# Kernel optimization log

Hardware: AMD Instinct MI355X
Metric: run time of the kernel (lower is better)

## Reference

```python
import jax, jax.numpy as jnp
import numpy as np

B, T, HID = 1, 8192, 2048
NH, NKV, D = 32, 8, 64
BLK, LOCAL, GLOB = 64, 8, 1
THETA = 10000.0
SCALE = 1.0 / float(np.sqrt(D))
NEG = -1e9


def _sparse_tables(nb):
    """Replicates HumanVAttention._get_sparse_tables: per query block i select
    global blocks [0, GLOB) then local blocks [i-LOCAL+1, i], dedup keeping order."""
    max_sel = LOCAL + GLOB
    idx = np.zeros((nb, max_sel), np.int32)
    valid = np.zeros((nb, max_sel), bool)
    for i in range(nb):
        sel = [g for g in range(GLOB) if g < nb]
        sel += list(range(max(0, i - (LOCAL - 1)), i + 1))
        li, seen = [], set()
        for x in sel:
            if x not in seen:
                li.append(x); seen.add(x)
        idx[i, :len(li)] = li
        valid[i, :len(li)] = True
    return idx, valid


def _rotate_half(x):
    x1, x2 = x[..., : x.shape[-1] // 2], x[..., x.shape[-1] // 2:]
    return jnp.concatenate((-x2, x1), axis=-1)


def setup_inputs() -> dict:
    key = jax.random.key(0)
    ks = jax.random.split(key, 5)
    s = 0.02
    return {
        "hidden_states": jax.random.normal(ks[0], (B, T, HID), jnp.float32),
        "Wq": jax.random.normal(ks[1], (NH * D, HID), jnp.float32) * s,
        "Wk": jax.random.normal(ks[2], (NKV * D, HID), jnp.float32) * s,
        "Wv": jax.random.normal(ks[3], (NKV * D, HID), jnp.float32) * s,
        "Wo": jax.random.normal(ks[4], (NH * D, NH * D), jnp.float32) * s,
    }


def reference(hidden_states, Wq, Wk, Wv, Wo):
    hs = hidden_states
    # projections (nn.Linear: y = x @ W.T)
    q = (hs @ Wq.T).reshape(B, T, NH, D).transpose(0, 2, 1, 3)     # [B,NH,T,D]
    k = (hs @ Wk.T).reshape(B, T, NKV, D).transpose(0, 2, 1, 3)    # [B,NKV,T,D]
    v = (hs @ Wv.T).reshape(B, T, NKV, D).transpose(0, 2, 1, 3)

    # RoPE (full rotary factor)
    inv = 1.0 / (THETA ** (jnp.arange(0, D, 2, dtype=jnp.float32) / D))
    fr = jnp.arange(T, dtype=jnp.float32)[:, None] * inv[None, :]  # [T,D/2]
    emb = jnp.concatenate([fr, fr], axis=-1)                       # [T,D]
    cos = jnp.cos(emb)[None, None]                                 # [1,1,T,D]
    sin = jnp.sin(emb)[None, None]
    q = q * cos + _rotate_half(q) * sin
    k = k * cos + _rotate_half(k) * sin

    nb = T // BLK
    G = NH // NKV
    idx_np, valid_np = _sparse_tables(nb)
    max_sel = idx_np.shape[1]

    # gather selected K/V blocks per query block
    kb = k.reshape(B, NKV, nb, BLK, D)
    vb = v.reshape(B, NKV, nb, BLK, D)
    idx = jnp.asarray(idx_np)
    k_sel = kb[:, :, idx].reshape(B, NKV, nb, max_sel * BLK, D)    # [B,NKV,nb,M,D]
    v_sel = vb[:, :, idx].reshape(B, NKV, nb, max_sel * BLK, D)

    qg = q.reshape(B, NKV, G, nb, BLK, D)                          # grouped queries
    scores = jnp.einsum('bkgnqd,bknmd->bkgnqm',
                        qg.astype(jnp.float32), k_sel.astype(jnp.float32)) * SCALE

    # causal + validity mask over selected keys (static, built in numpy)
    kpos = (idx_np[:, :, None] * BLK + np.arange(BLK)).reshape(nb, -1)   # [nb,M]
    qpos = np.arange(nb)[:, None] * BLK + np.arange(BLK)                 # [nb,BLK]
    valid_flat = np.repeat(valid_np, BLK, axis=1)                        # [nb,M]
    allowed = valid_flat[:, None, :] & (kpos[:, None, :] <= qpos[:, :, None])
    scores = jnp.where(jnp.asarray(allowed)[None, None, None], scores, NEG)

    probs = jax.nn.softmax(scores, axis=-1)
    out = jnp.einsum('bkgnqm,bknmd->bkgnqd', probs.astype(v.dtype), v_sel)
    out = out.astype(hs.dtype).reshape(B, NH, T, D).transpose(0, 2, 1, 3)
    out = out.reshape(B, T, NH * D)
    return out @ Wo.T
```

## Files before the change

### kernel.cpp

```cpp
#include <hip/hip_runtime.h>
#include <cstdint>
#include <cstddef>

typedef __bf16 bf16;
typedef __attribute__((ext_vector_type(8))) __bf16 bf16x8;
typedef __attribute__((ext_vector_type(4))) __bf16 bf16x4;
typedef __attribute__((ext_vector_type(4))) float f32x4;

#define ATT_SCALE 0.125f
#define NEG_BIG  -1000000000.0f

__device__ __forceinline__ f32x4 mfma16(bf16x8 a, bf16x8 b, f32x4 c) {
  return __builtin_amdgcn_mfma_f32_16x16x32_bf16(a, b, c, 0, 0, 0);
}

__device__ __forceinline__ void gload16(const bf16* g, bf16* l) {
  __builtin_amdgcn_global_load_lds((__attribute__((address_space(1))) void*)g,
                                   (__attribute__((address_space(3))) void*)l,
                                   16, 0, 0);
}

__global__ __launch_bounds__(256) void prep_all(const float* __restrict__ hs,
                                                const float* __restrict__ Wq,
                                                const float* __restrict__ Wk,
                                                const float* __restrict__ Wv,
                                                const float* __restrict__ Wo,
                                                bf16* __restrict__ hs16, bf16* __restrict__ wq16,
                                                bf16* __restrict__ wk16, bf16* __restrict__ wv16,
                                                bf16* __restrict__ wo16,
                                                float* __restrict__ cosT, float* __restrict__ sinT) {
  int b = blockIdx.x, t = threadIdx.x;
  const float* src; bf16* dst; int i;
  if (b < 16384)      { src = hs; dst = hs16; i = b * 256 + t; }
  else if (b < 20480) { src = Wq; dst = wq16; i = (b - 16384) * 256 + t; }
  else if (b < 21504) { src = Wk; dst = wk16; i = (b - 20480) * 256 + t; }
  else if (b < 22528) { src = Wv; dst = wv16; i = (b - 21504) * 256 + t; }
  else if (b < 26624) { src = Wo; dst = wo16; i = (b - 22528) * 256 + t; }
  else {
    int idx = (b - 26624) * 256 + t;
    int tt = idx >> 5, j = idx & 31;
    float inv = exp2f(-(float)j * (13.287712379549449f / 32.0f));
    float fr = (float)tt * inv;
    cosT[idx] = cosf(fr); sinT[idx] = sinf(fr);
    return;
  }
  float4 v = *((const float4*)src + i);
  bf16x4 o;
  o[0] = (bf16)v.x; o[1] = (bf16)v.y; o[2] = (bf16)v.z; o[3] = (bf16)v.w;
  *((bf16x4*)dst + i) = o;
}

template <int BSEL, int OUTF32, int ROPE>
__global__ __launch_bounds__(512, 2) void gemm256(const bf16* __restrict__ A,
                                                  const bf16* __restrict__ B0,
                                                  const bf16* __restrict__ B1,
                                                  const bf16* __restrict__ B2,
                                                  void* __restrict__ Cout,
                                                  const float* __restrict__ cosT,
                                                  const float* __restrict__ sinT,
                                                  int N, int K) {
  __shared__ bf16 Asm[4][8192];
  __shared__ bf16 Bsm[4][8192];
  const int tid = threadIdx.x, lane = tid & 63, wid = tid >> 6;
  const int m0 = blockIdx.x * 256, n0 = blockIdx.y * 256;
  const int wr = wid >> 2, wc = wid & 3;
  const int fr = lane & 15, g4 = lane >> 4;
  const int sw8 = (g4 ^ ((fr >> 1) & 3)) * 8;

  f32x4 acc[8][4] = {};

  auto brow = [&](int n) -> const bf16* {
    if (BSEL) {
      if (n < 2048) return B0 + (size_t)n * K;
      if (n < 2560) return B1 + (size_t)(n - 2048) * K;
      return B2 + (size_t)(n - 2560) * K;
    }
    return B0 + (size_t)n * K;
  };

  const bf16* aS0; const bf16* aS1; const bf16* bS0; const bf16* bS1;
  {
    int c0 = tid, r0 = c0 >> 2, l0 = (c0 & 3) ^ ((r0 >> 1) & 3);
    int c1 = 512 + tid, r1 = c1 >> 2, l1 = (c1 & 3) ^ ((r1 >> 1) & 3);
    aS0 = A + (size_t)(m0 + r0) * K + l0 * 8;
    aS1 = A + (size_t)(m0 + r1) * K + l1 * 8;
    bS0 = brow(n0 + r0) + l0 * 8;
    bS1 = brow(n0 + r1) + l1 * 8;
  }
  const int dst0 = (wid * 64) * 8;
  const int dst1 = (512 + wid * 64) * 8;

#define STAGE_A(kt) { bf16* d = &Asm[(kt) & 3][0]; \
    gload16(aS0 + (kt) * 32, d + dst0); gload16(aS1 + (kt) * 32, d + dst1); }
#define STAGE_B(kt) { bf16* d = &Bsm[(kt) & 3][0]; \
    gload16(bS0 + (kt) * 32, d + dst0); gload16(bS1 + (kt) * 32, d + dst1); }

#define KTILE(kt, VM, STG) { \
    asm volatile("s_waitcnt vmcnt(" VM ")" ::: "memory"); \
    __builtin_amdgcn_s_barrier(); \
    __builtin_amdgcn_sched_barrier(0); \
    const bf16* Ab = &Asm[(kt) & 3][0]; \
    const bf16* Bb = &Bsm[(kt) & 3][0]; \
    bf16x8 bfr[4], af[4]; \
    _Pragma("unroll") for (int nf = 0; nf < 4; ++nf) \
      bfr[nf] = *(const bf16x8*)(Bb + (wc * 64 + nf * 16 + fr) * 32 + sw8); \
    _Pragma("unroll") for (int mf = 0; mf < 4; ++mf) \
      af[mf] = *(const bf16x8*)(Ab + (wr * 128 + mf * 16 + fr) * 32 + sw8); \
    if (STG) STAGE_A((kt) + 3); \
    __builtin_amdgcn_s_setprio(1); \
    _Pragma("unroll") for (int mf = 0; mf < 4; ++mf) \
      _Pragma("unroll") for (int nf = 0; nf < 4; ++nf) \
        acc[mf][nf] = mfma16(af[mf], bfr[nf], acc[mf][nf]); \
    __builtin_amdgcn_s_setprio(0); \
    _Pragma("unroll") for (int mf = 0; mf < 4; ++mf) \
      af[mf] = *(const bf16x8*)(Ab + (wr * 128 + 64 + mf * 16 + fr) * 32 + sw8); \
    if (STG) STAGE_B((kt) + 3); \
    __builtin_amdgcn_s_setprio(1); \
    _Pragma("unroll") for (int mf = 0; mf < 4; ++mf) \
      _Pragma("unroll") for (int nf = 0; nf < 4; ++nf) \
        acc[4 + mf][nf] = mfma16(af[mf], bfr[nf], acc[4 + mf][nf]); \
    __builtin_amdgcn_s_setprio(0); \
  }

  STAGE_A(0); STAGE_B(0);
  STAGE_A(1); STAGE_B(1);
  STAGE_A(2); STAGE_B(2);

  const int NT = K >> 5;
  for (int kt = 0; kt < NT - 3; ++kt) KTILE(kt, "8", 1);
  KTILE(NT - 3, "8", 0);
  KTILE(NT - 2, "4", 0);
  KTILE(NT - 1, "0", 0);
#undef KTILE
#undef STAGE_A
#undef STAGE_B

  const int fc = lane & 15, fr4 = (lane >> 4) * 4;
  if (ROPE && (n0 + wc * 64) < 2560) {
#pragma unroll
    for (int am = 0; am < 8; ++am)
#pragma unroll
      for (int i = 0; i < 4; ++i) {
        size_t row = (size_t)(m0 + wr * 128 + am * 16 + fr4 + i);
        bf16* base = (bf16*)Cout + row * (size_t)N + n0 + wc * 64;
#pragma unroll
        for (int nf = 0; nf < 2; ++nf) {
          int j = nf * 16 + fc;
          float c = cosT[row * 32 + j], sn = sinT[row * 32 + j];
          float x1 = acc[am][nf][i], x2 = acc[am][nf + 2][i];
          base[j]      = (bf16)(x1 * c - x2 * sn);
          base[j + 32] = (bf16)(x2 * c + x1 * sn);
        }
      }
  } else {
#pragma unroll
    for (int am = 0; am < 8; ++am)
#pragma unroll
      for (int i = 0; i < 4; ++i) {
        size_t row = (size_t)(m0 + wr * 128 + am * 16 + fr4 + i);
#pragma unroll
        for (int nf = 0; nf < 4; ++nf) {
          int col = n0 + wc * 64 + nf * 16 + fc;
          if (OUTF32)
            ((float*)Cout)[row * (size_t)N + col] = acc[am][nf][i];
          else
            ((bf16*)Cout)[row * (size_t)N + col] = (bf16)acc[am][nf][i];
        }
      }
  }
}

__global__ __launch_bounds__(1024) void attn_sparse(const bf16* __restrict__ qkv,
                                                    bf16* __restrict__ attn) {
  const int iblk = blockIdx.x;
  const int kv = blockIdx.y;
  const int tid = threadIdx.x, lane = tid & 63, wid = tid >> 6;
  const int hloc = wid >> 2;
  const int h = kv * 4 + hloc;
  const int rg = wid & 3;

  __shared__ bf16 Ks[64 * 64];
  __shared__ bf16 Vt[2][64 * 72];
  __shared__ bf16 Ps[16 * 16 * 68];

  const int qcol = h * 64, kcol = 2048 + kv * 64, vcol = 2560 + kv * 64;
  const size_t trow0 = (size_t)iblk * 64;
  const int fr = lane & 15, g4 = lane >> 4, fk = g4 * 8, fr4 = g4 * 4;

  const bf16* qrow = qkv + (trow0 + rg * 16 + fr) * 3072 + qcol;
  bf16x8 bq0 = *(const bf16x8*)(qrow + fk);
  bf16x8 bq1 = *(const bf16x8*)(qrow + 32 + fk);

  float mrun = -INFINITY, lrun = 0.f;
  f32x4 acc[4] = {};

  const int kr = tid >> 3, ks = tid & 7;
  const int vu = tid & 511, vp = vu & 31, vd0 = (vu >> 5) * 4;
  const bool isK = (tid < 512);

  const int nsel = (iblk < 8) ? (iblk + 1) : 9;
  auto jof = [&](int js) { return (iblk < 8) ? js : ((js == 0) ? 0 : iblk - 8 + js); };

  {
    const size_t krow = (size_t)jof(0) * 64;
    if (isK) {
      const bf16* src = qkv + (krow + kr) * 3072 + kcol + ((ks ^ (kr & 7)) * 8);
      gload16(src, Ks + (tid >> 6) * 512);
    } else {
      const bf16* v0p = qkv + (krow + 2 * vp) * 3072 + vcol + vd0;
      uint64_t a = *(const uint64_t*)v0p;
      uint64_t b = *(const uint64_t*)(v0p + 3072);
#pragma unroll
      for (int e = 0; e < 4; ++e) {
        uint32_t w = (uint32_t)((a >> (16 * e)) & 0xFFFF) |
                     ((uint32_t)((b >> (16 * e)) & 0xFFFF) << 16);
        *(uint32_t*)(&Vt[0][0] + (vd0 + e) * 72 + 2 * vp) = w;
      }
    }
  }
  __syncthreads();

  for (int js = 0; js < nsel; ++js) {
    const int cur = js & 1;
    const int jblk = jof(js);
    const bool pre = (js + 1 < nsel);

    uint64_t va = 0, vb2 = 0;
    if (pre && !isK) {
      const bf16* v0p = qkv + ((size_t)jof(js + 1) * 64 + 2 * vp) * 3072 + vcol + vd0;
      va = *(const uint64_t*)v0p;
      vb2 = *(const uint64_t*)(v0p + 3072);
    }

    f32x4 s[4];
#pragma unroll
    for (int n = 0; n < 4; ++n) {
      const char* krowp = (const char*)Ks + (n * 16 + fr) * 128;
      bf16x8 kb0 = *(const bf16x8*)(krowp + ((g4 ^ (fr & 7)) << 4));
      bf16x8 kb1 = *(const bf16x8*)(krowp + (((4 + g4) ^ (fr & 7)) << 4));
      f32x4 z = {};
      z = mfma16(kb0, bq0, z);
      s[n] = mfma16(kb1, bq1, z);
    }

    __syncthreads();
    if (pre && isK) {
      const bf16* src = qkv + ((size_t)jof(js + 1) * 64 + kr) * 3072 + kcol +
                        ((ks ^ (kr & 7)) * 8);
      gload16(src, Ks + (tid >> 6) * 512);
    }

    const bool diag = (jblk == iblk);
    const int qr = rg * 16 + fr;
#pragma unroll
    for (int n = 0; n < 4; ++n)
#pragma unroll
      for (int i = 0; i < 4; ++i) {
        float sv = s[n][i] * ATT_SCALE;
        if (diag && (n * 16 + fr4 + i) > qr) sv = NEG_BIG;
        s[n][i] = sv;
      }

    float t0 = fmaxf(fmaxf(s[0][0], s[0][1]), fmaxf(s[0][2], s[0][3]));
    float t1 = fmaxf(fmaxf(s[1][0], s[1][1]), fmaxf(s[1][2], s[1][3]));
    float t2 = fmaxf(fmaxf(s[2][0], s[2][1]), fmaxf(s[2][2], s[2][3]));
    float t3 = fmaxf(fmaxf(s[3][0], s[3][1]), fmaxf(s[3][2], s[3][3]));
    float mx = fmaxf(fmaxf(t0, t1), fmaxf(t2, t3));
    mx = fmaxf(mx, __shfl_xor(mx, 16, 64));
    mx = fmaxf(mx, __shfl_xor(mx, 32, 64));
    float mnew = fmaxf(mrun, mx);
    float corr = __expf(mrun - mnew);
    mrun = mnew;
    float ps = 0.f;
#pragma unroll
    for (int n = 0; n < 4; ++n) {
      float p0 = __expf(s[n][0] - mnew), p1 = __expf(s[n][1] - mnew);
      float p2 = __expf(s[n][2] - mnew), p3 = __expf(s[n][3] - mnew);
      s[n][0] = p0; s[n][1] = p1; s[n][2] = p2; s[n][3] = p3;
      ps += (p0 + p1) + (p2 + p3);
    }
    ps += __shfl_xor(ps, 16, 64);
    ps += __shfl_xor(ps, 32, 64);
    lrun = lrun * corr + ps;

    float cq[4];
#pragma unroll
    for (int i = 0; i < 4; ++i) cq[i] = __shfl(corr, fr4 + i, 64);
#pragma unroll
    for (int n = 0; n < 4; ++n)
#pragma unroll
      for (int i = 0; i < 4; ++i) acc[n][i] *= cq[i];

    bf16* pbase = Ps + wid * (16 * 68);
#pragma unroll
    for (int n = 0; n < 4; ++n) {
      bf16x4 pk;
#pragma unroll
      for (int i = 0; i < 4; ++i) pk[i] = (bf16)s[n][i];
      *(bf16x4*)(pbase + fr * 68 + n * 16 + fr4) = pk;
    }
    bf16x8 pa0 = *(const bf16x8*)(pbase + fr * 68 + fk);
    bf16x8 pa1 = *(const bf16x8*)(pbase + fr * 68 + 32 + fk);

    if (pre && !isK) {
#pragma unroll
      for (int e = 0; e < 4; ++e) {
        uint32_t w = (uint32_t)((va >> (16 * e)) & 0xFFFF) |
                     ((uint32_t)((vb2 >> (16 * e)) & 0xFFFF) << 16);
        *(uint32_t*)(&Vt[cur ^ 1][0] + (vd0 + e) * 72 + 2 * vp) = w;
      }
    }

#pragma unroll
    for (int n = 0; n < 4; ++n) {
      bf16x8 vb0 = *(const bf16x8*)(&Vt[cur][0] + (n * 16 + fr) * 72 + fk);
      bf16x8 vb1 = *(const bf16x8*)(&Vt[cur][0] + (n * 16 + fr) * 72 + 32 + fk);
      acc[n] = mfma16(pa0, vb0, acc[n]);
      acc[n] = mfma16(pa1, vb1, acc[n]);
    }
    __syncthreads();
  }

  float lq[4];
#pragma unroll
  for (int i = 0; i < 4; ++i) lq[i] = __shfl(lrun, fr4 + i, 64);
#pragma unroll
  for (int i = 0; i < 4; ++i) {
    float rl = 1.0f / lq[i];
    size_t t = trow0 + rg * 16 + fr4 + i;
#pragma unroll
    for (int n = 0; n < 4; ++n)
      attn[t * 2048 + h * 64 + n * 16 + fr] = (bf16)(acc[n][i] * rl);
  }
}

extern "C" void kernel_launch(void* const* d_in, const int* in_sizes, int n_in,
                              void* d_out, int out_size, void* d_ws, size_t ws_size,
                              hipStream_t stream) {
  (void)in_sizes; (void)n_in; (void)out_size; (void)ws_size;
  const float* hs = (const float*)d_in[0];
  const float* Wq = (const float*)d_in[1];
  const float* Wk = (const float*)d_in[2];
  const float* Wv = (const float*)d_in[3];
  const float* Wo = (const float*)d_in[4];
  float* out = (float*)d_out;

  char* ws = (char*)d_ws;
  bf16* hs16 = (bf16*)(ws + 0);
  bf16* qkv  = (bf16*)(ws + 33554432);
  bf16* attn = (bf16*)(ws + 83886080);
  bf16* wq16 = (bf16*)(ws + 117440512);
  bf16* wk16 = (bf16*)(ws + 125829120);
  bf16* wv16 = (bf16*)(ws + 127926272);
  bf16* wo16 = (bf16*)(ws + 130023424);
  float* cosT = (float*)(ws + 138412032);
  float* sinT = (float*)(ws + 139460608);

  prep_all<<<27648, 256, 0, stream>>>(hs, Wq, Wk, Wv, Wo,
                                      hs16, wq16, wk16, wv16, wo16, cosT, sinT);

  gemm256<1, 0, 1><<<dim3(32, 12), 512, 0, stream>>>(hs16, wq16, wk16, wv16, qkv,
                                                     cosT, sinT, 3072, 2048);
  attn_sparse<<<dim3(128, 8), 1024, 0, stream>>>(qkv, attn);
  gemm256<0, 1, 0><<<dim3(32, 8), 512, 0, stream>>>(attn, wo16, wo16, wo16, out,
                                                    nullptr, nullptr, 2048, 2048);
}
```

Baseline: 319.4 us.

## Restructure GEMM mainloop into ping-pong double-buffered phases with XCD-aware block remap

Changes the 256x256 GEMM main loop from a 4-stage ring of K=32 tiles into two K=64 buffers, each split into two K halves. The work runs as eight phases per 128-wide K step, each with a barrier, a single global-to-LDS stage, and 16 MFMAs, with explicit lgkmcnt/vmcnt waits. It also remaps the linear block id so consecutive tiles are spread across the eight XCDs, which is meant to improve L2 locality. The extra barriers per phase could add sync overhead, and the remap assumes the tile count divides by 8.

```diff
diff --git a/kernel.cpp b/kernel.cpp
--- a/kernel.cpp
+++ b/kernel.cpp
@@ -59,10 +59,16 @@
                                                   const float* __restrict__ cosT,
                                                   const float* __restrict__ sinT,
                                                   int N, int K) {
-  __shared__ bf16 Asm[4][8192];
-  __shared__ bf16 Bsm[4][8192];
+  __shared__ bf16 As[2][2][8192];
+  __shared__ bf16 Bs[2][2][8192];
   const int tid = threadIdx.x, lane = tid & 63, wid = tid >> 6;
-  const int m0 = blockIdx.x * 256, n0 = blockIdx.y * 256;
+
+  const int nx = gridDim.x;
+  int lin = blockIdx.x + nx * blockIdx.y;
+  const int cpx = (nx * gridDim.y) >> 3;
+  lin = (lin & 7) * cpx + (lin >> 3);
+  const int m0 = (lin % nx) * 256, n0 = (lin / nx) * 256;
+
   const int wr = wid >> 2, wc = wid & 3;
   const int fr = lane & 15, g4 = lane >> 4;
   const int sw8 = (g4 ^ ((fr >> 1) & 3)) * 8;
@@ -78,60 +84,79 @@
     return B0 + (size_t)n * K;
   };
 
-  const bf16* aS0; const bf16* aS1; const bf16* bS0; const bf16* bS1;
-  {
-    int c0 = tid, r0 = c0 >> 2, l0 = (c0 & 3) ^ ((r0 >> 1) & 3);
-    int c1 = 512 + tid, r1 = c1 >> 2, l1 = (c1 & 3) ^ ((r1 >> 1) & 3);
-    aS0 = A + (size_t)(m0 + r0) * K + l0 * 8;
-    aS1 = A + (size_t)(m0 + r1) * K + l1 * 8;
-    bS0 = brow(n0 + r0) + l0 * 8;
-    bS1 = brow(n0 + r1) + l1 * 8;
-  }
-  const int dst0 = (wid * 64) * 8;
-  const int dst1 = (512 + wid * 64) * 8;
-
-#define STAGE_A(kt) { bf16* d = &Asm[(kt) & 3][0]; \
-    gload16(aS0 + (kt) * 32, d + dst0); gload16(aS1 + (kt) * 32, d + dst1); }
-#define STAGE_B(kt) { bf16* d = &Bsm[(kt) & 3][0]; \
-    gload16(bS0 + (kt) * 32, d + dst0); gload16(bS1 + (kt) * 32, d + dst1); }
-
-#define KTILE(kt, VM, STG) { \
-    asm volatile("s_waitcnt vmcnt(" VM ")" ::: "memory"); \
+  const int r0 = tid >> 2, r1 = 128 + (tid >> 2);
+  const int l0 = (tid & 3) ^ ((r0 >> 1) & 3);
+  const int l1 = (tid & 3) ^ ((r1 >> 1) & 3);
+  const bf16* aS0 = A + (size_t)(m0 + r0) * K + l0 * 8;
+  const bf16* aS1 = A + (size_t)(m0 + r1) * K + l1 * 8;
+  const bf16* bS0 = brow(n0 + r0) + l0 * 8;
+  const bf16* bS1 = brow(n0 + r1) + l1 * 8;
+  const int st0 = wid * 512;
+  const int st1 = 4096 + wid * 512;
+
+#define STAGE_A(BUF, KH, KT) { \
+    gload16(aS0 + (KT) * 64 + (KH) * 32, &As[BUF][KH][0] + st0); \
+    gload16(aS1 + (KT) * 64 + (KH) * 32, &As[BUF][KH][0] + st1); }
+#define STAGE_B(BUF, KH, KT) { \
+    gload16(bS0 + (KT) * 64 + (KH) * 32, &Bs[BUF][KH][0] + st0); \
+    gload16(bS1 + (KT) * 64 + (KH) * 32, &Bs[BUF][KH][0] + st1); }
+#define VMX {}
+#define VM4 { asm volatile("s_waitcnt vmcnt(4)" ::: "memory"); }
+#define VM0 { asm volatile("s_waitcnt vmcnt(0)" ::: "memory"); }
+
+#define PHASE(BUF, KK, MH, LOADB, STG, VM) { \
+    if (LOADB) { \
+      _Pragma("unroll") for (int nf = 0; nf < 4; ++nf) \
+        bfr[nf] = *(const bf16x8*)(&Bs[BUF][KK][0] + (wc * 64 + nf * 16 + fr) * 32 + sw8); \
+    } \
+    bf16x8 af[4]; \
+    _Pragma("unroll") for (int mf = 0; mf < 4; ++mf) \
+      af[mf] = *(const bf16x8*)(&As[BUF][KK][0] + (wr * 128 + (MH) * 64 + mf * 16 + fr) * 32 + sw8); \
+    STG \
     __builtin_amdgcn_s_barrier(); \
+    asm volatile("s_waitcnt lgkmcnt(0)" ::: "memory"); \
     __builtin_amdgcn_sched_barrier(0); \
-    const bf16* Ab = &Asm[(kt) & 3][0]; \
-    const bf16* Bb = &Bsm[(kt) & 3][0]; \
-    bf16x8 bfr[4], af[4]; \
-    _Pragma("unroll") for (int nf = 0; nf < 4; ++nf) \
-      bfr[nf] = *(const bf16x8*)(Bb + (wc * 64 + nf * 16 + fr) * 32 + sw8); \
-    _Pragma("unroll") for (int mf = 0; mf < 4; ++mf) \
-      af[mf] = *(const bf16x8*)(Ab + (wr * 128 + mf * 16 + fr) * 32 + sw8); \
-    if (STG) STAGE_A((kt) + 3); \
     __builtin_amdgcn_s_setprio(1); \
     _Pragma("unroll") for (int mf = 0; mf < 4; ++mf) \
       _Pragma("unroll") for (int nf = 0; nf < 4; ++nf) \
-        acc[mf][nf] = mfma16(af[mf], bfr[nf], acc[mf][nf]); \
+        acc[(MH) * 4 + mf][nf] = mfma16(af[mf], bfr[nf], acc[(MH) * 4 + mf][nf]); \
     __builtin_amdgcn_s_setprio(0); \
-    _Pragma("unroll") for (int mf = 0; mf < 4; ++mf) \
-      af[mf] = *(const bf16x8*)(Ab + (wr * 128 + 64 + mf * 16 + fr) * 32 + sw8); \
-    if (STG) STAGE_B((kt) + 3); \
-    __builtin_amdgcn_s_setprio(1); \
-    _Pragma("unroll") for (int mf = 0; mf < 4; ++mf) \
-      _Pragma("unroll") for (int nf = 0; nf < 4; ++nf) \
-        acc[4 + mf][nf] = mfma16(af[mf], bfr[nf], acc[4 + mf][nf]); \
-    __builtin_amdgcn_s_setprio(0); \
-  }
-
-  STAGE_A(0); STAGE_B(0);
-  STAGE_A(1); STAGE_B(1);
-  STAGE_A(2); STAGE_B(2);
-
-  const int NT = K >> 5;
-  for (int kt = 0; kt < NT - 3; ++kt) KTILE(kt, "8", 1);
-  KTILE(NT - 3, "8", 0);
-  KTILE(NT - 2, "4", 0);
-  KTILE(NT - 1, "0", 0);
-#undef KTILE
+    VM \
+    __builtin_amdgcn_s_barrier(); \
+    __builtin_amdgcn_sched_barrier(0); }
+
+  STAGE_A(0, 0, 0); STAGE_B(0, 0, 0);
+  STAGE_A(0, 1, 0); STAGE_B(0, 1, 0);
+  STAGE_A(1, 0, 1); STAGE_B(1, 0, 1);
+  asm volatile("s_waitcnt vmcnt(4)" ::: "memory");
+  __builtin_amdgcn_s_barrier();
+
+  const int NI = K >> 7;
+  for (int i = 0; i < NI - 1; ++i) {
+    const int kt = 2 * i;
+    bf16x8 bfr[4];
+    PHASE(0, 0, 0, 1, STAGE_A(1, 1, kt + 1), VMX)
+    PHASE(0, 0, 1, 0, STAGE_B(1, 1, kt + 1), VM4)
+    PHASE(0, 1, 0, 1, STAGE_A(0, 0, kt + 2), VMX)
+    PHASE(0, 1, 1, 0, STAGE_B(0, 0, kt + 2), VM4)
+    PHASE(1, 0, 0, 1, STAGE_A(0, 1, kt + 2), VMX)
+    PHASE(1, 0, 1, 0, STAGE_B(0, 1, kt + 2), VM4)
+    PHASE(1, 1, 0, 1, STAGE_A(1, 0, kt + 3), VMX)
+    PHASE(1, 1, 1, 0, STAGE_B(1, 0, kt + 3), VM4)
+  }
+  {
+    const int kt = 2 * (NI - 1);
+    bf16x8 bfr[4];
+    PHASE(0, 0, 0, 1, STAGE_A(1, 1, kt + 1), VMX)
+    PHASE(0, 0, 1, 0, STAGE_B(1, 1, kt + 1), VM4)
+    PHASE(0, 1, 0, 1, {}, VMX)
+    PHASE(0, 1, 1, 0, {}, VM0)
+    PHASE(1, 0, 0, 1, {}, VMX)
+    PHASE(1, 0, 1, 0, {}, VMX)
+    PHASE(1, 1, 0, 1, {}, VMX)
+    PHASE(1, 1, 1, 0, {}, VMX)
+  }
+#undef PHASE
 #undef STAGE_A
 #undef STAGE_B
 
@@ -141,7 +166,7 @@
     for (int am = 0; am < 8; ++am)
 #pragma unroll
       for (int i = 0; i < 4; ++i) {
-        size_t row = (size_t)(m0 + wr * 128 + am * 16 + fr4 + i);
+        size_t row = (size_t)(m0 + wr * 128 + (am >> 2) * 64 + (am & 3) * 16 + fr4 + i);
         bf16* base = (bf16*)Cout + row * (size_t)N + n0 + wc * 64;
 #pragma unroll
         for (int nf = 0; nf < 2; ++nf) {
@@ -157,7 +182,7 @@
     for (int am = 0; am < 8; ++am)
 #pragma unroll
       for (int i = 0; i < 4; ++i) {
-        size_t row = (size_t)(m0 + wr * 128 + am * 16 + fr4 + i);
+        size_t row = (size_t)(m0 + wr * 128 + (am >> 2) * 64 + (am & 3) * 16 + fr4 + i);
 #pragma unroll
         for (int nf = 0; nf < 4; ++nf) {
           int col = n0 + wc * 64 + nf * 16 + fc;
```

After: 362.2 us. 13.4% more time.

## Load GEMM B operand directly into registers, dropping its LDS staging

Applied to the files above, without the earlier changes.

The B tile is no longer staged through shared memory with async global-to-LDS loads. Each wave now loads its B fragments straight from global memory into double-buffered registers, one k-tile ahead. Only A stays in the 4-stage LDS ring. This halves LDS footprint and LDS traffic, which could allow higher occupancy. The cost is that B reuse across waves is lost: each wave row re-reads the same B columns from global or L2. Prefetching only one tile ahead may also expose load latency, and the vmcnt accounting changes.

```diff
diff --git a/kernel.cpp b/kernel.cpp
--- a/kernel.cpp
+++ b/kernel.cpp
@@ -59,10 +59,10 @@
                                                   const float* __restrict__ cosT,
                                                   const float* __restrict__ sinT,
                                                   int N, int K) {
-  __shared__ bf16 Asm[4][8192];
-  __shared__ bf16 Bsm[4][8192];
+  __shared__ bf16 As[4][8192];
   const int tid = threadIdx.x, lane = tid & 63, wid = tid >> 6;
   const int m0 = blockIdx.x * 256, n0 = blockIdx.y * 256;
+
   const int wr = wid >> 2, wc = wid & 3;
   const int fr = lane & 15, g4 = lane >> 4;
   const int sw8 = (g4 ^ ((fr >> 1) & 3)) * 8;
@@ -78,62 +78,67 @@
     return B0 + (size_t)n * K;
   };
 
-  const bf16* aS0; const bf16* aS1; const bf16* bS0; const bf16* bS1;
-  {
-    int c0 = tid, r0 = c0 >> 2, l0 = (c0 & 3) ^ ((r0 >> 1) & 3);
-    int c1 = 512 + tid, r1 = c1 >> 2, l1 = (c1 & 3) ^ ((r1 >> 1) & 3);
-    aS0 = A + (size_t)(m0 + r0) * K + l0 * 8;
-    aS1 = A + (size_t)(m0 + r1) * K + l1 * 8;
-    bS0 = brow(n0 + r0) + l0 * 8;
-    bS1 = brow(n0 + r1) + l1 * 8;
-  }
-  const int dst0 = (wid * 64) * 8;
-  const int dst1 = (512 + wid * 64) * 8;
-
-#define STAGE_A(kt) { bf16* d = &Asm[(kt) & 3][0]; \
-    gload16(aS0 + (kt) * 32, d + dst0); gload16(aS1 + (kt) * 32, d + dst1); }
-#define STAGE_B(kt) { bf16* d = &Bsm[(kt) & 3][0]; \
-    gload16(bS0 + (kt) * 32, d + dst0); gload16(bS1 + (kt) * 32, d + dst1); }
-
-#define KTILE(kt, VM, STG) { \
+  const int r0 = tid >> 2, r1 = 128 + (tid >> 2);
+  const int l0 = (tid & 3) ^ ((r0 >> 1) & 3);
+  const int l1 = (tid & 3) ^ ((r1 >> 1) & 3);
+  const bf16* aS0 = A + (size_t)(m0 + r0) * K + l0 * 8;
+  const bf16* aS1 = A + (size_t)(m0 + r1) * K + l1 * 8;
+  const int st0 = wid * 512;
+  const int st1 = 4096 + wid * 512;
+
+  const bf16* bp[4];
+#pragma unroll
+  for (int nf = 0; nf < 4; ++nf)
+    bp[nf] = brow(n0 + wc * 64 + nf * 16 + fr) + g4 * 8;
+
+  bf16x8 bA[4], bB[4];
+
+#define STAGE_A(KT) { \
+    gload16(aS0 + (KT) * 32, &As[(KT) & 3][0] + st0); \
+    gload16(aS1 + (KT) * 32, &As[(KT) & 3][0] + st1); }
+
+#define TILE(KT, BCUR, BNXT, VM, STG, PF) { \
     asm volatile("s_waitcnt vmcnt(" VM ")" ::: "memory"); \
     __builtin_amdgcn_s_barrier(); \
     __builtin_amdgcn_sched_barrier(0); \
-    const bf16* Ab = &Asm[(kt) & 3][0]; \
-    const bf16* Bb = &Bsm[(kt) & 3][0]; \
-    bf16x8 bfr[4], af[4]; \
-    _Pragma("unroll") for (int nf = 0; nf < 4; ++nf) \
-      bfr[nf] = *(const bf16x8*)(Bb + (wc * 64 + nf * 16 + fr) * 32 + sw8); \
+    const bf16* Ab = &As[(KT) & 3][0]; \
+    bf16x8 af[4]; \
     _Pragma("unroll") for (int mf = 0; mf < 4; ++mf) \
       af[mf] = *(const bf16x8*)(Ab + (wr * 128 + mf * 16 + fr) * 32 + sw8); \
-    if (STG) STAGE_A((kt) + 3); \
+    if (PF) { _Pragma("unroll") for (int nf = 0; nf < 4; ++nf) \
+      BNXT[nf] = *(const bf16x8*)(bp[nf] + ((KT) + 1) * 32); } \
+    if (STG) STAGE_A((KT) + 3); \
     __builtin_amdgcn_s_setprio(1); \
     _Pragma("unroll") for (int mf = 0; mf < 4; ++mf) \
       _Pragma("unroll") for (int nf = 0; nf < 4; ++nf) \
-        acc[mf][nf] = mfma16(af[mf], bfr[nf], acc[mf][nf]); \
+        acc[mf][nf] = mfma16(af[mf], BCUR[nf], acc[mf][nf]); \
     __builtin_amdgcn_s_setprio(0); \
     _Pragma("unroll") for (int mf = 0; mf < 4; ++mf) \
       af[mf] = *(const bf16x8*)(Ab + (wr * 128 + 64 + mf * 16 + fr) * 32 + sw8); \
-    if (STG) STAGE_B((kt) + 3); \
     __builtin_amdgcn_s_setprio(1); \
     _Pragma("unroll") for (int mf = 0; mf < 4; ++mf) \
       _Pragma("unroll") for (int nf = 0; nf < 4; ++nf) \
-        acc[4 + mf][nf] = mfma16(af[mf], bfr[nf], acc[4 + mf][nf]); \
+        acc[4 + mf][nf] = mfma16(af[mf], BCUR[nf], acc[4 + mf][nf]); \
     __builtin_amdgcn_s_setprio(0); \
   }
 
-  STAGE_A(0); STAGE_B(0);
-  STAGE_A(1); STAGE_B(1);
-  STAGE_A(2); STAGE_B(2);
+  STAGE_A(0);
+#pragma unroll
+  for (int nf = 0; nf < 4; ++nf) bA[nf] = *(const bf16x8*)(bp[nf]);
+  STAGE_A(1);
+  STAGE_A(2);
 
   const int NT = K >> 5;
-  for (int kt = 0; kt < NT - 3; ++kt) KTILE(kt, "8", 1);
-  KTILE(NT - 3, "8", 0);
-  KTILE(NT - 2, "4", 0);
-  KTILE(NT - 1, "0", 0);
-#undef KTILE
+  TILE(0, bA, bB, "4", 1, 1)
+  for (int kt = 1; kt + 2 < NT - 1; kt += 2) {
+    TILE(kt, bB, bA, "2", 1, 1)
+    TILE(kt + 1, bA, bB, "2", 1, 1)
+  }
+  TILE(NT - 3, bB, bA, "2", 0, 1)
+  TILE(NT - 2, bA, bB, "0", 0, 1)
+  TILE(NT - 1, bB, bA, "0", 0, 0)
+#undef TILE
 #undef STAGE_A
-#undef STAGE_B
 
   const int fc = lane & 15, fr4 = (lane >> 4) * 4;
   if (ROPE && (n0 + wc * 64) < 2560) {
```

Result: slower. 425.6 us (+33.2%).

## Use 256x384 tiles with triple buffering for fused QKV GEMM

Applied to the files above, without the earlier changes.

The QKV projection now runs in a dedicated kernel with 256x384 output tiles, so the grid is 32x8 = 256 blocks instead of 384. That matches one wave of blocks on the 256 CUs and removes the partial second wave. Each block uses a 2x4 warp layout with 64x192 per warp and a 3-stage LDS ring buffer instead of 4 stages, with RoPE applied per 64-column group in the epilogue. The output projection becomes a specialised non-template copy of the old GEMM. The cost is more accumulator registers per thread (48 f32x4) and the loss of the two-blocks-per-CU launch bound, which lowers occupancy.

```diff
diff --git a/kernel.cpp b/kernel.cpp
--- a/kernel.cpp
+++ b/kernel.cpp
@@ -50,33 +50,137 @@
   *((bf16x4*)dst + i) = o;
 }
 
-template <int BSEL, int OUTF32, int ROPE>
-__global__ __launch_bounds__(512, 2) void gemm256(const bf16* __restrict__ A,
-                                                  const bf16* __restrict__ B0,
-                                                  const bf16* __restrict__ B1,
-                                                  const bf16* __restrict__ B2,
-                                                  void* __restrict__ Cout,
-                                                  const float* __restrict__ cosT,
-                                                  const float* __restrict__ sinT,
-                                                  int N, int K) {
-  __shared__ bf16 Asm[4][8192];
-  __shared__ bf16 Bsm[4][8192];
+__global__ __launch_bounds__(512) void gemm_qkv(const bf16* __restrict__ A,
+                                                const bf16* __restrict__ B0,
+                                                const bf16* __restrict__ B1,
+                                                const bf16* __restrict__ B2,
+                                                bf16* __restrict__ C,
+                                                const float* __restrict__ cosT,
+                                                const float* __restrict__ sinT) {
+  __shared__ bf16 As[3][8192];
+  __shared__ bf16 Bs[3][12288];
+  const int tid = threadIdx.x, lane = tid & 63, wid = tid >> 6;
+  const int m0 = blockIdx.x * 256, n0 = blockIdx.y * 384;
+  const int wr = wid >> 1, wc = wid & 1;
+  const int fr = lane & 15, g4 = lane >> 4;
+  const int sw8 = (g4 ^ ((fr >> 1) & 3)) * 8;
+
+  f32x4 acc[4][12] = {};
+
+  auto brow = [&](int n) -> const bf16* {
+    if (n < 2048) return B0 + (size_t)n * 2048;
+    if (n < 2560) return B1 + (size_t)(n - 2048) * 2048;
+    return B2 + (size_t)(n - 2560) * 2048;
+  };
+
+  const int ra0 = tid >> 2, ra1 = 128 + (tid >> 2), rb2r = 256 + (tid >> 2);
+  const bf16* aS0 = A + (size_t)(m0 + ra0) * 2048 + ((tid & 3) ^ ((ra0 >> 1) & 3)) * 8;
+  const bf16* aS1 = A + (size_t)(m0 + ra1) * 2048 + ((tid & 3) ^ ((ra1 >> 1) & 3)) * 8;
+  const bf16* bS0 = brow(n0 + ra0) + ((tid & 3) ^ ((ra0 >> 1) & 3)) * 8;
+  const bf16* bS1 = brow(n0 + ra1) + ((tid & 3) ^ ((ra1 >> 1) & 3)) * 8;
+  const bf16* bS2 = brow(n0 + rb2r) + ((tid & 3) ^ ((rb2r >> 1) & 3)) * 8;
+  const int d0 = wid * 512, d1 = 4096 + wid * 512, d2 = 8192 + wid * 512;
+
+#define STQA(BS, KT)  { bf16* d = &As[BS][0]; \
+    gload16(aS0 + (KT) * 32, d + d0); gload16(aS1 + (KT) * 32, d + d1); }
+#define STQB0(BS, KT) { bf16* d = &Bs[BS][0]; \
+    gload16(bS0 + (KT) * 32, d + d0); gload16(bS1 + (KT) * 32, d + d1); }
+#define STQB1(BS, KT) { gload16(bS2 + (KT) * 32, &Bs[BS][0] + d2); }
+
+#define QTILE(KT, BI, BS, VM, STG) { \
+    asm volatile("s_waitcnt vmcnt(" VM ")" ::: "memory"); \
+    __builtin_amdgcn_s_barrier(); \
+    __builtin_amdgcn_sched_barrier(0); \
+    const bf16* Ab = &As[BI][0]; \
+    const bf16* Bb = &Bs[BI][0]; \
+    bf16x8 af[4], bfr[4]; \
+    _Pragma("unroll") for (int mf = 0; mf < 4; ++mf) \
+      af[mf] = *(const bf16x8*)(Ab + (wr * 64 + mf * 16 + fr) * 32 + sw8); \
+    _Pragma("unroll") for (int q = 0; q < 4; ++q) \
+      bfr[q] = *(const bf16x8*)(Bb + (wc * 192 + q * 16 + fr) * 32 + sw8); \
+    if (STG) STQA(BS, (KT) + 2); \
+    __builtin_amdgcn_s_setprio(1); \
+    _Pragma("unroll") for (int mf = 0; mf < 4; ++mf) \
+      _Pragma("unroll") for (int q = 0; q < 4; ++q) \
+        acc[mf][q] = mfma16(af[mf], bfr[q], acc[mf][q]); \
+    __builtin_amdgcn_s_setprio(0); \
+    _Pragma("unroll") for (int q = 0; q < 4; ++q) \
+      bfr[q] = *(const bf16x8*)(Bb + (wc * 192 + 64 + q * 16 + fr) * 32 + sw8); \
+    if (STG) STQB0(BS, (KT) + 2); \
+    __builtin_amdgcn_s_setprio(1); \
+    _Pragma("unroll") for (int mf = 0; mf < 4; ++mf) \
+      _Pragma("unroll") for (int q = 0; q < 4; ++q) \
+        acc[mf][4 + q] = mfma16(af[mf], bfr[q], acc[mf][4 + q]); \
+    __builtin_amdgcn_s_setprio(0); \
+    _Pragma("unroll") for (int q = 0; q < 4; ++q) \
+      bfr[q] = *(const bf16x8*)(Bb + (wc * 192 + 128 + q * 16 + fr) * 32 + sw8); \
+    if (STG) STQB1(BS, (KT) + 2); \
+    __builtin_amdgcn_s_setprio(1); \
+    _Pragma("unroll") for (int mf = 0; mf < 4; ++mf) \
+      _Pragma("unroll") for (int q = 0; q < 4; ++q) \
+        acc[mf][8 + q] = mfma16(af[mf], bfr[q], acc[mf][8 + q]); \
+    __builtin_amdgcn_s_setprio(0); \
+  }
+
+  STQA(0, 0); STQB0(0, 0); STQB1(0, 0);
+  STQA(1, 1); STQB0(1, 1); STQB1(1, 1);
+
+  int bi = 0, bs = 2;
+  for (int kt = 0; kt < 62; ++kt) {
+    QTILE(kt, bi, bs, "5", 1)
+    bi = (bi == 2) ? 0 : bi + 1;
+    bs = (bs == 2) ? 0 : bs + 1;
+  }
+  QTILE(62, bi, bs, "5", 0)
+  bi = (bi == 2) ? 0 : bi + 1;
+  QTILE(63, bi, bi, "0", 0)
+#undef QTILE
+#undef STQA
+#undef STQB0
+#undef STQB1
+
+  const int fc = lane & 15, fr4 = (lane >> 4) * 4;
+#pragma unroll
+  for (int mf = 0; mf < 4; ++mf)
+#pragma unroll
+    for (int i = 0; i < 4; ++i) {
+      size_t row = (size_t)(m0 + wr * 64 + mf * 16 + fr4 + i);
+      bf16* base = C + row * 3072 + n0 + wc * 192;
+      const float* cr = cosT + row * 32;
+      const float* sr = sinT + row * 32;
+#pragma unroll
+      for (int g = 0; g < 3; ++g) {
+        if (n0 + wc * 192 + g * 64 < 2560) {
+#pragma unroll
+          for (int q = 0; q < 2; ++q) {
+            int j = q * 16 + fc;
+            float c = cr[j], sn = sr[j];
+            float x1 = acc[mf][g * 4 + q][i], x2 = acc[mf][g * 4 + q + 2][i];
+            base[g * 64 + j]      = (bf16)(x1 * c - x2 * sn);
+            base[g * 64 + j + 32] = (bf16)(x2 * c + x1 * sn);
+          }
+        } else {
+#pragma unroll
+          for (int q = 0; q < 4; ++q)
+            base[g * 64 + q * 16 + fc] = (bf16)acc[mf][g * 4 + q][i];
+        }
+      }
+    }
+}
+
+__global__ __launch_bounds__(512, 2) void gemm_out(const bf16* __restrict__ A,
+                                                   const bf16* __restrict__ B0,
+                                                   float* __restrict__ Cout) {
+  __shared__ bf16 As[4][8192];
+  __shared__ bf16 Bs[4][8192];
   const int tid = threadIdx.x, lane = tid & 63, wid = tid >> 6;
   const int m0 = blockIdx.x * 256, n0 = blockIdx.y * 256;
   const int wr = wid >> 2, wc = wid & 3;
   const int fr = lane & 15, g4 = lane >> 4;
   const int sw8 = (g4 ^ ((fr >> 1) & 3)) * 8;
+  const int K = 2048, N = 2048;
 
   f32x4 acc[8][4] = {};
-
-  auto brow = [&](int n) -> const bf16* {
-    if (BSEL) {
-      if (n < 2048) return B0 + (size_t)n * K;
-      if (n < 2560) return B1 + (size_t)(n - 2048) * K;
-      return B2 + (size_t)(n - 2560) * K;
-    }
-    return B0 + (size_t)n * K;
-  };
 
   const bf16* aS0; const bf16* aS1; const bf16* bS0; const bf16* bS1;
   {
@@ -84,29 +188,29 @@
     int c1 = 512 + tid, r1 = c1 >> 2, l1 = (c1 & 3) ^ ((r1 >> 1) & 3);
     aS0 = A + (size_t)(m0 + r0) * K + l0 * 8;
     aS1 = A + (size_t)(m0 + r1) * K + l1 * 8;
-    bS0 = brow(n0 + r0) + l0 * 8;
-    bS1 = brow(n0 + r1) + l1 * 8;
-  }
-  const int dst0 = (wid * 64) * 8;
-  const int dst1 = (512 + wid * 64) * 8;
-
-#define STAGE_A(kt) { bf16* d = &Asm[(kt) & 3][0]; \
-    gload16(aS0 + (kt) * 32, d + dst0); gload16(aS1 + (kt) * 32, d + dst1); }
-#define STAGE_B(kt) { bf16* d = &Bsm[(kt) & 3][0]; \
-    gload16(bS0 + (kt) * 32, d + dst0); gload16(bS1 + (kt) * 32, d + dst1); }
-
-#define KTILE(kt, VM, STG) { \
+    bS0 = B0 + (size_t)(n0 + r0) * K + l0 * 8;
+    bS1 = B0 + (size_t)(n0 + r1) * K + l1 * 8;
+  }
+  const int dst0 = wid * 512;
+  const int dst1 = 4096 + wid * 512;
+
+#define STAGE_A(KT) { bf16* d = &As[(KT) & 3][0]; \
+    gload16(aS0 + (KT) * 32, d + dst0); gload16(aS1 + (KT) * 32, d + dst1); }
+#define STAGE_B(KT) { bf16* d = &Bs[(KT) & 3][0]; \
+    gload16(bS0 + (KT) * 32, d + dst0); gload16(bS1 + (KT) * 32, d + dst1); }
+
+#define KTILE(KT, VM, STG) { \
     asm volatile("s_waitcnt vmcnt(" VM ")" ::: "memory"); \
     __builtin_amdgcn_s_barrier(); \
     __builtin_amdgcn_sched_barrier(0); \
-    const bf16* Ab = &Asm[(kt) & 3][0]; \
-    const bf16* Bb = &Bsm[(kt) & 3][0]; \
+    const bf16* Ab = &As[(KT) & 3][0]; \
+    const bf16* Bb = &Bs[(KT) & 3][0]; \
     bf16x8 bfr[4], af[4]; \
     _Pragma("unroll") for (int nf = 0; nf < 4; ++nf) \
       bfr[nf] = *(const bf16x8*)(Bb + (wc * 64 + nf * 16 + fr) * 32 + sw8); \
     _Pragma("unroll") for (int mf = 0; mf < 4; ++mf) \
       af[mf] = *(const bf16x8*)(Ab + (wr * 128 + mf * 16 + fr) * 32 + sw8); \
-    if (STG) STAGE_A((kt) + 3); \
+    if (STG) STAGE_A((KT) + 3); \
     __builtin_amdgcn_s_setprio(1); \
     _Pragma("unroll") for (int mf = 0; mf < 4; ++mf) \
       _Pragma("unroll") for (int nf = 0; nf < 4; ++nf) \
@@ -114,7 +218,7 @@
     __builtin_amdgcn_s_setprio(0); \
     _Pragma("unroll") for (int mf = 0; mf < 4; ++mf) \
       af[mf] = *(const bf16x8*)(Ab + (wr * 128 + 64 + mf * 16 + fr) * 32 + sw8); \
-    if (STG) STAGE_B((kt) + 3); \
+    if (STG) STAGE_B((KT) + 3); \
     __builtin_amdgcn_s_setprio(1); \
     _Pragma("unroll") for (int mf = 0; mf < 4; ++mf) \
       _Pragma("unroll") for (int nf = 0; nf < 4; ++nf) \
@@ -127,47 +231,26 @@
   STAGE_A(2); STAGE_B(2);
 
   const int NT = K >> 5;
-  for (int kt = 0; kt < NT - 3; ++kt) KTILE(kt, "8", 1);
-  KTILE(NT - 3, "8", 0);
-  KTILE(NT - 2, "4", 0);
-  KTILE(NT - 1, "0", 0);
+  for (int kt = 0; kt < NT - 3; ++kt) KTILE(kt, "8", 1)
+  KTILE(NT - 3, "8", 0)
+  KTILE(NT - 2, "4", 0)
+  KTILE(NT - 1, "0", 0)
 #undef KTILE
 #undef STAGE_A
 #undef STAGE_B
 
   const int fc = lane & 15, fr4 = (lane >> 4) * 4;
-  if (ROPE && (n0 + wc * 64) < 2560) {
-#pragma unroll
-    for (int am = 0; am < 8; ++am)
-#pragma unroll
-      for (int i = 0; i < 4; ++i) {
-        size_t row = (size_t)(m0 + wr * 128 + am * 16 + fr4 + i);
-        bf16* base = (bf16*)Cout + row * (size_t)N + n0 + wc * 64;
-#pragma unroll
-        for (int nf = 0; nf < 2; ++nf) {
-          int j = nf * 16 + fc;
-          float c = cosT[row * 32 + j], sn = sinT[row * 32 + j];
-          float x1 = acc[am][nf][i], x2 = acc[am][nf + 2][i];
-          base[j]      = (bf16)(x1 * c - x2 * sn);
-          base[j + 32] = (bf16)(x2 * c + x1 * sn);
-        }
+#pragma unroll
+  for (int am = 0; am < 8; ++am)
+#pragma unroll
+    for (int i = 0; i < 4; ++i) {
+      size_t row = (size_t)(m0 + wr * 128 + am * 16 + fr4 + i);
+#pragma unroll
+      for (int nf = 0; nf < 4; ++nf) {
+        int col = n0 + wc * 64 + nf * 16 + fc;
+        Cout[row * (size_t)N + col] = acc[am][nf][i];
       }
-  } else {
-#pragma unroll
-    for (int am = 0; am < 8; ++am)
-#pragma unroll
-      for (int i = 0; i < 4; ++i) {
-        size_t row = (size_t)(m0 + wr * 128 + am * 16 + fr4 + i);
-#pragma unroll
-        for (int nf = 0; nf < 4; ++nf) {
-          int col = n0 + wc * 64 + nf * 16 + fc;
-          if (OUTF32)
-            ((float*)Cout)[row * (size_t)N + col] = acc[am][nf][i];
-          else
-            ((bf16*)Cout)[row * (size_t)N + col] = (bf16)acc[am][nf][i];
-        }
-      }
-  }
+    }
 }
 
 __global__ __launch_bounds__(1024) void attn_sparse(const bf16* __restrict__ qkv,
@@ -359,9 +442,7 @@
   prep_all<<<27648, 256, 0, stream>>>(hs, Wq, Wk, Wv, Wo,
                                       hs16, wq16, wk16, wv16, wo16, cosT, sinT);
 
-  gemm256<1, 0, 1><<<dim3(32, 12), 512, 0, stream>>>(hs16, wq16, wk16, wv16, qkv,
-                                                     cosT, sinT, 3072, 2048);
+  gemm_qkv<<<dim3(32, 8), 512, 0, stream>>>(hs16, wq16, wk16, wv16, qkv, cosT, sinT);
   attn_sparse<<<dim3(128, 8), 1024, 0, stream>>>(qkv, attn);
-  gemm256<0, 1, 0><<<dim3(32, 8), 512, 0, stream>>>(attn, wo16, wo16, wo16, out,
-                                                    nullptr, nullptr, 2048, 2048);
-}
+  gemm_out<<<dim3(32, 8), 512, 0, stream>>>(attn, wo16, out);
+}
```

After: 299.6 us. 1.07x faster.
